# Kernel tuning notes

Hardware: AMD Instinct MI355X
Metric: run time of the kernel (lower is better)

The kernel has to match this reference:

```python
import jax, jax.numpy as jnp
import numpy as np

B, S, H, I = 128, 197, 768, 3072
EPS = 1e-12


def _binarize_ste(x):
    # forward: sign(x); backward: clipped straight-through (grad where |x|<=1)
    xc = jnp.clip(x, -1.0, 1.0)
    return xc + jax.lax.stop_gradient(jnp.sign(x) - xc)


def setup_inputs() -> dict:
    key = jax.random.key(0)
    ks = jax.random.split(key, 4)
    return {
        "hidden_states": jax.random.normal(ks[0], (B, S, H), dtype=jnp.float32),
        "W": jax.random.normal(ks[1], (I, H), dtype=jnp.float32) * 0.02,
        "b": jax.random.normal(ks[2], (I,), dtype=jnp.float32) * 0.02,
        "move": jnp.zeros((H,), dtype=jnp.float32),
        "ln_gamma": jnp.ones((I,), dtype=jnp.float32),
        "ln_beta": jnp.zeros((I,), dtype=jnp.float32),
        "move1": jnp.zeros((I,), dtype=jnp.float32),
        "prelu_alpha": jnp.full((I,), 0.25, dtype=jnp.float32),
        "move2": jnp.zeros((I,), dtype=jnp.float32),
    }


def reference(hidden_states, W, b, move, ln_gamma, ln_beta, move1, prelu_alpha, move2):
    # QuantizeLinear: 1-bit weights scaled by per-row mean(|W|), 1-bit activations
    alpha_w = jnp.mean(jnp.abs(W), axis=1, keepdims=True)      # [I,1]
    bw = alpha_w * _binarize_ste(W)                            # [I,H]
    xb = _binarize_ste(hidden_states + move)                   # [B,S,H]
    y = jnp.einsum("bsh,ih->bsi", xb, bw) + b                  # [B,S,I]

    # LayerNorm over intermediate dim
    mu = jnp.mean(y, axis=-1, keepdims=True)
    var = jnp.mean(jnp.square(y - mu), axis=-1, keepdims=True)
    yn = (y - mu) * jax.lax.rsqrt(var + EPS) * ln_gamma + ln_beta

    res = jnp.concatenate([hidden_states] * 4, axis=-1)        # [B,S,I]
    out = yn + res

    # RPReLU: per-feature PReLU (transpose trick in torch == channel=last dim)
    z = out - move1
    out = jnp.where(z >= 0, z, prelu_alpha * z) + move2
    return out
```

## Files before the change

kernel.cpp:

```cpp
#include <hip/hip_runtime.h>
#include <stdint.h>

#define HDIM 768
#define IDIM 3072
#define NROWS 25216
#define RPB 8
#define TPB 512
#define KCH 6

__global__ __launch_bounds__(256) void wprep_kernel(
    const float* __restrict__ W, const float* __restrict__ bias,
    uint32_t* __restrict__ wbits, float* __restrict__ c0, float* __restrict__ c1)
{
    const int wv   = threadIdx.x >> 6;
    const int lane = threadIdx.x & 63;
    const int i    = blockIdx.x * 4 + wv;
    const float* wr = W + (size_t)i * HDIM;

    float sabs = 0.f;
    uint32_t myword = 0;
    #pragma unroll
    for (int c = 0; c < 12; ++c) {
        float w = wr[c * 64 + lane];
        sabs += fabsf(w);
        unsigned long long mask = __ballot(w > 0.f);
        if (lane == 2 * c)     myword = (uint32_t)mask;
        if (lane == 2 * c + 1) myword = (uint32_t)(mask >> 32);
    }
    #pragma unroll
    for (int m = 32; m; m >>= 1) sabs += __shfl_xor(sabs, m, 64);

    if (lane < 24)
        wbits[(size_t)i * 24 + lane] = myword;
    if (lane == 0) {
        c0[i] = sabs + bias[i];
        c1[i] = sabs * (2.0f / 768.0f);
    }
}

__global__ __launch_bounds__(256) void xprep_kernel(
    const float* __restrict__ hid, const float* __restrict__ move,
    uint32_t* __restrict__ xbits)
{
    const int wv   = threadIdx.x >> 6;
    const int lane = threadIdx.x & 63;
    const int row  = blockIdx.x * 4 + wv;
    const float* hr = hid + (size_t)row * HDIM;

    uint32_t myword = 0;
    #pragma unroll
    for (int j = 0; j < 12; ++j) {
        int h = j * 64 + lane;
        float v = hr[h] + move[h];
        unsigned long long mask = __ballot(v > 0.f);
        if (lane == 2 * j)     myword = (uint32_t)mask;
        if (lane == 2 * j + 1) myword = (uint32_t)(mask >> 32);
    }
    if (lane < 24) xbits[(size_t)row * 24 + lane] = myword;
}

__global__ __launch_bounds__(TPB) void fused_kernel(
    const float* __restrict__ hid,
    const uint32_t* __restrict__ xbits,
    const uint32_t* __restrict__ wbits,
    const float* __restrict__ c0, const float* __restrict__ c1,
    const float* __restrict__ gamma, const float* __restrict__ beta,
    const float* __restrict__ move1, const float* __restrict__ pal,
    const float* __restrict__ move2, float* __restrict__ out)
{
    __shared__ float hlds[RPB * HDIM];
    __shared__ float red[8][RPB][2];
    __shared__ float musd[RPB][2];

    const int tid  = threadIdx.x;
    const int wv   = tid >> 6;
    const int lane = tid & 63;
    const size_t row0 = (size_t)blockIdx.x * RPB;

    {
        const float4* src = (const float4*)(hid + row0 * HDIM);
        float4* dst = (float4*)hlds;
        #pragma unroll
        for (int p = 0; p < 3; ++p) dst[tid + p * TPB] = src[tid + p * TPB];
    }

    const uint4* xb4 = (const uint4*)(xbits + row0 * 24);

    float y[KCH][RPB];
    #pragma unroll
    for (int k = 0; k < KCH; ++k) {
        asm volatile("" ::: "memory");
        const int i = k * TPB + tid;
        uint32_t wb[24];
        {
            const uint4* wp = (const uint4*)(wbits + (size_t)i * 24);
            #pragma unroll
            for (int wg = 0; wg < 6; ++wg) {
                uint4 v = wp[wg];
                wb[4*wg+0] = v.x; wb[4*wg+1] = v.y;
                wb[4*wg+2] = v.z; wb[4*wg+3] = v.w;
            }
        }
        const float C0 = c0[i], C1 = c1[i];
        #pragma unroll
        for (int r = 0; r < RPB; ++r) {
            int m = 0;
            #pragma unroll
            for (int wg = 0; wg < 6; ++wg) {
                uint4 x = xb4[r * 6 + wg];
                m += __popc(wb[4*wg+0] ^ x.x);
                m += __popc(wb[4*wg+1] ^ x.y);
                m += __popc(wb[4*wg+2] ^ x.z);
                m += __popc(wb[4*wg+3] ^ x.w);
            }
            y[k][r] = C0 - C1 * (float)m;
        }
    }

    #pragma unroll
    for (int r = 0; r < RPB; ++r) {
        float s = 0.f, q = 0.f;
        #pragma unroll
        for (int k = 0; k < KCH; ++k) { float v = y[k][r]; s += v; q += v * v; }
        #pragma unroll
        for (int m = 32; m; m >>= 1) {
            s += __shfl_xor(s, m, 64);
            q += __shfl_xor(q, m, 64);
        }
        if (lane == 0) { red[wv][r][0] = s; red[wv][r][1] = q; }
    }
    __syncthreads();
    if (tid < 64) {
        const int r = tid >> 3, w = tid & 7;
        float s = red[w][r][0], q = red[w][r][1];
        #pragma unroll
        for (int m = 1; m < 8; m <<= 1) {
            s += __shfl_xor(s, m, 64);
            q += __shfl_xor(q, m, 64);
        }
        if (w == 0) {
            float mu  = s * (1.0f / 3072.0f);
            float var = q * (1.0f / 3072.0f) - mu * mu;
            musd[r][0] = mu;
            musd[r][1] = rsqrtf(var + 1e-12f);
        }
    }
    __syncthreads();

    float mur[RPB], rsr[RPB];
    #pragma unroll
    for (int r = 0; r < RPB; ++r) { mur[r] = musd[r][0]; rsr[r] = musd[r][1]; }

    #pragma unroll
    for (int k = 0; k < KCH; ++k) {
        const int i = k * TPB + tid;
        const float g  = gamma[i], be = beta[i];
        const float m1 = move1[i], pa = pal[i], m2 = move2[i];
        const int h = i % HDIM;
        #pragma unroll
        for (int r = 0; r < RPB; ++r) {
            float yn = (y[k][r] - mur[r]) * rsr[r] * g + be;
            float o  = yn + hlds[r * HDIM + h];
            float z  = o - m1;
            o = (z >= 0.f ? z : pa * z) + m2;
            out[(row0 + r) * IDIM + i] = o;
        }
    }
}

extern "C" void kernel_launch(void* const* d_in, const int* in_sizes, int n_in,
                              void* d_out, int out_size, void* d_ws, size_t ws_size,
                              hipStream_t stream)
{
    const float* hs    = (const float*)d_in[0];
    const float* W     = (const float*)d_in[1];
    const float* bias  = (const float*)d_in[2];
    const float* move  = (const float*)d_in[3];
    const float* gamma = (const float*)d_in[4];
    const float* beta  = (const float*)d_in[5];
    const float* move1 = (const float*)d_in[6];
    const float* pal   = (const float*)d_in[7];
    const float* move2 = (const float*)d_in[8];
    float* out = (float*)d_out;

    uint32_t* xbits = (uint32_t*)d_ws;
    uint32_t* wbits = xbits + (size_t)NROWS * 24;
    float*    c0    = (float*)(wbits + (size_t)IDIM * 24);
    float*    c1    = c0 + IDIM;

    wprep_kernel<<<IDIM / 4, 256, 0, stream>>>(W, bias, wbits, c0, c1);
    xprep_kernel<<<NROWS / 4, 256, 0, stream>>>(hs, move, xbits);
    fused_kernel<<<NROWS / RPB, TPB, 0, stream>>>(
        hs, xbits, wbits, c0, c1, gamma, beta, move1, pal, move2, out);
}
```

Before: 663.9 us.

## Fuse activation binarization into main kernel and restructure popcount loop order

Removes the separate xprep kernel. Each block now binarizes its 8 rows straight from the hidden-state tile already staged in LDS, using wave ballots, and writes the bit masks to shared memory. This saves the extra kernel launch plus the global write and re-read of xbits. The popcount loop is also reordered so weight-bit chunks stream in per 128-bit group while x bits are reused from LDS. The trade-off is more integer accumulators held live in registers, an extra barrier, and more loads of the weight bits.

```diff
diff --git a/kernel.cpp b/kernel.cpp
--- a/kernel.cpp
+++ b/kernel.cpp
@@ -38,30 +38,8 @@
     }
 }
 
-__global__ __launch_bounds__(256) void xprep_kernel(
+__global__ __launch_bounds__(TPB) void fused_kernel(
     const float* __restrict__ hid, const float* __restrict__ move,
-    uint32_t* __restrict__ xbits)
-{
-    const int wv   = threadIdx.x >> 6;
-    const int lane = threadIdx.x & 63;
-    const int row  = blockIdx.x * 4 + wv;
-    const float* hr = hid + (size_t)row * HDIM;
-
-    uint32_t myword = 0;
-    #pragma unroll
-    for (int j = 0; j < 12; ++j) {
-        int h = j * 64 + lane;
-        float v = hr[h] + move[h];
-        unsigned long long mask = __ballot(v > 0.f);
-        if (lane == 2 * j)     myword = (uint32_t)mask;
-        if (lane == 2 * j + 1) myword = (uint32_t)(mask >> 32);
-    }
-    if (lane < 24) xbits[(size_t)row * 24 + lane] = myword;
-}
-
-__global__ __launch_bounds__(TPB) void fused_kernel(
-    const float* __restrict__ hid,
-    const uint32_t* __restrict__ xbits,
     const uint32_t* __restrict__ wbits,
     const float* __restrict__ c0, const float* __restrict__ c1,
     const float* __restrict__ gamma, const float* __restrict__ beta,
@@ -69,6 +47,7 @@
     const float* __restrict__ move2, float* __restrict__ out)
 {
     __shared__ float hlds[RPB * HDIM];
+    __shared__ __attribute__((aligned(16))) uint32_t xlds[RPB][24];
     __shared__ float red[8][RPB][2];
     __shared__ float musd[RPB][2];
 
@@ -83,64 +62,81 @@
         #pragma unroll
         for (int p = 0; p < 3; ++p) dst[tid + p * TPB] = src[tid + p * TPB];
     }
+    __syncthreads();
 
-    const uint4* xb4 = (const uint4*)(xbits + row0 * 24);
+    #pragma unroll
+    for (int j = 0; j < 12; ++j) {
+        int h = j * 64 + lane;
+        float v = hlds[wv * HDIM + h] + move[h];
+        unsigned long long mask = __ballot(v > 0.f);
+        if (lane == 0) xlds[wv][2 * j]     = (uint32_t)mask;
+        if (lane == 1) xlds[wv][2 * j + 1] = (uint32_t)(mask >> 32);
+    }
+    __syncthreads();
+
+    int m[KCH][RPB];
+    #pragma unroll
+    for (int k = 0; k < KCH; ++k)
+        #pragma unroll
+        for (int r = 0; r < RPB; ++r) m[k][r] = 0;
+
+    #pragma unroll
+    for (int wg = 0; wg < 6; ++wg) {
+        uint4 xr[RPB];
+        #pragma unroll
+        for (int r = 0; r < RPB; ++r)
+            xr[r] = *(const uint4*)&xlds[r][wg * 4];
+        #pragma unroll
+        for (int k = 0; k < KCH; ++k) {
+            const int i = k * TPB + tid;
+            uint4 wb = *(const uint4*)(wbits + (size_t)i * 24 + wg * 4);
+            #pragma unroll
+            for (int r = 0; r < RPB; ++r) {
+                m[k][r] += __popc(wb.x ^ xr[r].x) + __popc(wb.y ^ xr[r].y)
+                         + __popc(wb.z ^ xr[r].z) + __popc(wb.w ^ xr[r].w);
+            }
+        }
+    }
 
     float y[KCH][RPB];
+    float s[RPB], q[RPB];
+    #pragma unroll
+    for (int r = 0; r < RPB; ++r) { s[r] = 0.f; q[r] = 0.f; }
     #pragma unroll
     for (int k = 0; k < KCH; ++k) {
-        asm volatile("" ::: "memory");
         const int i = k * TPB + tid;
-        uint32_t wb[24];
-        {
-            const uint4* wp = (const uint4*)(wbits + (size_t)i * 24);
-            #pragma unroll
-            for (int wg = 0; wg < 6; ++wg) {
-                uint4 v = wp[wg];
-                wb[4*wg+0] = v.x; wb[4*wg+1] = v.y;
-                wb[4*wg+2] = v.z; wb[4*wg+3] = v.w;
-            }
-        }
         const float C0 = c0[i], C1 = c1[i];
         #pragma unroll
         for (int r = 0; r < RPB; ++r) {
-            int m = 0;
-            #pragma unroll
-            for (int wg = 0; wg < 6; ++wg) {
-                uint4 x = xb4[r * 6 + wg];
-                m += __popc(wb[4*wg+0] ^ x.x);
-                m += __popc(wb[4*wg+1] ^ x.y);
-                m += __popc(wb[4*wg+2] ^ x.z);
-                m += __popc(wb[4*wg+3] ^ x.w);
-            }
-            y[k][r] = C0 - C1 * (float)m;
+            float v = C0 - C1 * (float)m[k][r];
+            y[k][r] = v;
+            s[r] += v;
+            q[r] += v * v;
         }
     }
 
     #pragma unroll
     for (int r = 0; r < RPB; ++r) {
-        float s = 0.f, q = 0.f;
+        float sr = s[r], qr = q[r];
         #pragma unroll
-        for (int k = 0; k < KCH; ++k) { float v = y[k][r]; s += v; q += v * v; }
-        #pragma unroll
-        for (int m = 32; m; m >>= 1) {
-            s += __shfl_xor(s, m, 64);
-            q += __shfl_xor(q, m, 64);
+        for (int mm = 32; mm; mm >>= 1) {
+            sr += __shfl_xor(sr, mm, 64);
+            qr += __shfl_xor(qr, mm, 64);
         }
-        if (lane == 0) { red[wv][r][0] = s; red[wv][r][1] = q; }
+        if (lane == 0) { red[wv][r][0] = sr; red[wv][r][1] = qr; }
     }
     __syncthreads();
     if (tid < 64) {
         const int r = tid >> 3, w = tid & 7;
-        float s = red[w][r][0], q = red[w][r][1];
+        float sr = red[w][r][0], qr = red[w][r][1];
         #pragma unroll
-        for (int m = 1; m < 8; m <<= 1) {
-            s += __shfl_xor(s, m, 64);
-            q += __shfl_xor(q, m, 64);
+        for (int mm = 1; mm < 8; mm <<= 1) {
+            sr += __shfl_xor(sr, mm, 64);
+            qr += __shfl_xor(qr, mm, 64);
         }
         if (w == 0) {
-            float mu  = s * (1.0f / 3072.0f);
-            float var = q * (1.0f / 3072.0f) - mu * mu;
+            float mu  = sr * (1.0f / 3072.0f);
+            float var = qr * (1.0f / 3072.0f) - mu * mu;
             musd[r][0] = mu;
             musd[r][1] = rsqrtf(var + 1e-12f);
         }
@@ -183,13 +179,11 @@
     const float* move2 = (const float*)d_in[8];
     float* out = (float*)d_out;
 
-    uint32_t* xbits = (uint32_t*)d_ws;
-    uint32_t* wbits = xbits + (size_t)NROWS * 24;
+    uint32_t* wbits = (uint32_t*)d_ws;
     float*    c0    = (float*)(wbits + (size_t)IDIM * 24);
     float*    c1    = c0 + IDIM;
 
     wprep_kernel<<<IDIM / 4, 256, 0, stream>>>(W, bias, wbits, c0, c1);
-    xprep_kernel<<<NROWS / 4, 256, 0, stream>>>(hs, move, xbits);
     fused_kernel<<<NROWS / RPB, TPB, 0, stream>>>(
-        hs, xbits, wbits, c0, c1, gamma, beta, move1, pal, move2, out);
+        hs, move, wbits, c0, c1, gamma, beta, move1, pal, move2, out);
 }
```

Result: slower. 1.049 ms (+58.0%).
